# Kernel tuning notes

Hardware: AMD Instinct MI355X
Metric: run time of the kernel (lower is better)

The kernel has to match this reference:

```python
import jax, jax.numpy as jnp
import numpy as np

N_NODES = 10000
N_EDGES = 640000
D_FEAT = 128


def setup_inputs() -> dict:
    key = jax.random.key(0)
    k1, k2, k3, k4 = jax.random.split(key, 4)
    feat = jax.random.normal(k1, (N_NODES, D_FEAT), dtype=jnp.float32)
    src = jax.random.randint(k2, (N_EDGES,), 0, N_NODES, dtype=jnp.int32)
    dst = jax.random.randint(k3, (N_EDGES,), 0, N_NODES, dtype=jnp.int32)
    W = jax.random.normal(k4, (D_FEAT, D_FEAT), dtype=jnp.float32) / np.sqrt(D_FEAT).astype(np.float32)
    b = jnp.zeros((D_FEAT,), dtype=jnp.float32)
    return {"feat": feat, "W": W, "b": b, "src": src, "dst": dst}


def reference(feat, W, b, src, dst):
    eps = jnp.float32(0.0)  # init_eps=0, learn_eps=False (buffer)
    n = feat.shape[0]
    # message passing: copy_u('h','m') + sum reducer -> neigh[i] = sum_{j->i} h_j
    h_src = feat[src]                                   # [E, D] gather
    neigh = jax.ops.segment_sum(h_src, dst, num_segments=n)  # [N, D] scatter-add
    rst = (1.0 + eps) * feat + neigh
    # apply_func: Linear(D, D)
    rst = rst @ W + b
    # per-edge score: e = sum(h_src * tanh(h_dst), axis=1)
    e = jnp.sum(h_src * jnp.tanh(feat[dst]), axis=1)    # [E]
    # edge_softmax: softmax over edges grouped by destination node
    m = jax.ops.segment_max(e, dst, num_segments=n)     # [N]
    e_exp = jnp.exp(e - m[dst])
    denom = jax.ops.segment_sum(e_exp, dst, num_segments=n)  # [N]
    e_soft = e_exp / denom[dst]
    return rst, e_soft
```

## Files before the change

kernel.cpp:

```cpp
#include <hip/hip_runtime.h>
#include <hip/hip_bf16.h>
#include <math.h>

#define N_NODES 10000
#define N_EDGES 640000
#define D_FEAT  128
#define SLOT    128
#define MAXDEG  128


__device__ __forceinline__ unsigned bf16rne2(float a, float b) {
    unsigned ua = __float_as_uint(a);
    unsigned ub = __float_as_uint(b);
    unsigned ra = (ua + 0x7fffu + ((ua >> 16) & 1u)) >> 16;
    unsigned rb = (ub + 0x7fffu + ((ub >> 16) & 1u)) >> 16;
    return ra | (rb << 16);
}

__global__ void scatter_build(const int* __restrict__ src,
                              const int* __restrict__ dst,
                              const float* __restrict__ feat,
                              int* __restrict__ cnt,
                              unsigned short* __restrict__ slot_us,
                              int* __restrict__ pos_by_edge,
                              unsigned short* __restrict__ feat_bf) {
    int tid = blockIdx.x * 256 + threadIdx.x;

    if (tid < (N_NODES * D_FEAT) / 8) {
        int t8 = tid * 8;
        float4 f0 = *(const float4*)&feat[t8];
        float4 f1 = *(const float4*)&feat[t8 + 4];
        uint4 p;
        p.x = bf16rne2(f0.x, f0.y);
        p.y = bf16rne2(f0.z, f0.w);
        p.z = bf16rne2(f1.x, f1.y);
        p.w = bf16rne2(f1.z, f1.w);
        *(uint4*)&feat_bf[t8] = p;
    }

    int d = dst[tid];
    int s = src[tid];
    int pos = atomicAdd(&cnt[d << 4], 1);
    int idx = d * SLOT + pos;
    slot_us[idx] = (unsigned short)s;
    pos_by_edge[tid] = idx;
}

__device__ __forceinline__ float cvt_acc_dot(uint4 U, float4 t0, float4 t1,
                                             float4& a0, float4& a1) {
    float v0 = __uint_as_float(U.x << 16);
    float v1 = __uint_as_float(U.x & 0xffff0000u);
    float v2 = __uint_as_float(U.y << 16);
    float v3 = __uint_as_float(U.y & 0xffff0000u);
    float v4 = __uint_as_float(U.z << 16);
    float v5 = __uint_as_float(U.z & 0xffff0000u);
    float v6 = __uint_as_float(U.w << 16);
    float v7 = __uint_as_float(U.w & 0xffff0000u);
    a0.x += v0; a0.y += v1; a0.z += v2; a0.w += v3;
    a1.x += v4; a1.y += v5; a1.z += v6; a1.w += v7;
    return v0 * t0.x + v1 * t0.y + v2 * t0.z + v3 * t0.w
         + v4 * t1.x + v5 * t1.y + v6 * t1.z + v7 * t1.w;
}

__global__ void fused_node(const float* __restrict__ feat,
                           const unsigned short* __restrict__ feat_bf,
                           const int* __restrict__ cnt,
                           const unsigned short* __restrict__ slot_us,
                           float* __restrict__ e_slot,
                           float* __restrict__ x_out) {
    __shared__ float t_sh[4][D_FEAT];
    __shared__ float e_sh[4][MAXDEG];
    int wv = threadIdx.x >> 6;
    int lane = threadIdx.x & 63;
    int node = blockIdx.x * 4 + wv;
    if (node >= N_NODES) return;

    int g = lane >> 4;
    int l = lane & 15;

    int deg = cnt[node << 4];
    int dm = (deg > 0) ? deg - 1 : 0;
    unsigned base = (unsigned)node * SLOT;

    float2 fd2 = ((const float2*)(feat + (size_t)node * D_FEAT))[lane];
    ((float2*)&t_sh[wv][0])[lane] = make_float2(tanhf(fd2.x), tanhf(fd2.y));
    float4 t0 = ((const float4*)&t_sh[wv][0])[l * 2];
    float4 t1 = ((const float4*)&t_sh[wv][0])[l * 2 + 1];

    int m0 = (int)slot_us[base + min(lane, dm)];
    int m1 = (int)slot_us[base + min(64 + lane, dm)];

    float4 acc0 = make_float4(0.f, 0.f, 0.f, 0.f);
    float4 acc1 = make_float4(0.f, 0.f, 0.f, 0.f);

    int nsteps = (deg + 7) >> 3;

    uint4 Ua0, Ua1;
    #define LOAD_STEP(T, U0, U1)                                              \
        {                                                                     \
            int m_ = ((T) < 8) ? m0 : m1;                                     \
            int s0_ = __shfl(m_, ((T) * 8 + g) & 63, 64);                     \
            int s1_ = __shfl(m_, ((T) * 8 + 4 + g) & 63, 64);                 \
            U0 = *((const uint4*)(feat_bf + (size_t)s0_ * D_FEAT) + l);       \
            U1 = *((const uint4*)(feat_bf + (size_t)s1_ * D_FEAT) + l);       \
        }

    if (nsteps > 0) LOAD_STEP(0, Ua0, Ua1);

    for (int t = 0; t < nsteps; ++t) {
        uint4 Ub0 = Ua0, Ub1 = Ua1;
        if (t + 1 < nsteps) LOAD_STEP(t + 1, Ub0, Ub1);

        int i0 = t * 8 + g;
        int i1 = i0 + 4;
        if (((t + 1) << 3) <= deg) {
            float d0 = cvt_acc_dot(Ua0, t0, t1, acc0, acc1);
            float d1 = cvt_acc_dot(Ua1, t0, t1, acc0, acc1);
            #pragma unroll
            for (int off = 1; off <= 8; off <<= 1) {
                d0 += __shfl_xor(d0, off, 64);
                d1 += __shfl_xor(d1, off, 64);
            }
            if (l == 0) {
                e_sh[wv][i0] = d0;
                e_sh[wv][i1] = d1;
            }
        } else {
            bool a0 = i0 < deg, a1 = i1 < deg;
            if (!a0) Ua0 = make_uint4(0u, 0u, 0u, 0u);
            if (!a1) Ua1 = make_uint4(0u, 0u, 0u, 0u);
            float d0 = cvt_acc_dot(Ua0, t0, t1, acc0, acc1);
            float d1 = cvt_acc_dot(Ua1, t0, t1, acc0, acc1);
            #pragma unroll
            for (int off = 1; off <= 8; off <<= 1) {
                d0 += __shfl_xor(d0, off, 64);
                d1 += __shfl_xor(d1, off, 64);
            }
            if (a0 && l == 0) e_sh[wv][i0] = d0;
            if (a1 && l == 0) e_sh[wv][i1] = d1;
        }
        Ua0 = Ub0; Ua1 = Ub1;
    }
    #undef LOAD_STEP

    #pragma unroll
    for (int off = 16; off <= 32; off <<= 1) {
        acc0.x += __shfl_xor(acc0.x, off, 64);
        acc0.y += __shfl_xor(acc0.y, off, 64);
        acc0.z += __shfl_xor(acc0.z, off, 64);
        acc0.w += __shfl_xor(acc0.w, off, 64);
        acc1.x += __shfl_xor(acc1.x, off, 64);
        acc1.y += __shfl_xor(acc1.y, off, 64);
        acc1.z += __shfl_xor(acc1.z, off, 64);
        acc1.w += __shfl_xor(acc1.w, off, 64);
    }

    float2 mp = (g == 0) ? make_float2(acc0.x, acc0.y)
              : (g == 1) ? make_float2(acc0.z, acc0.w)
              : (g == 2) ? make_float2(acc1.x, acc1.y)
              :            make_float2(acc1.z, acc1.w);
    int p2 = l * 4 + g;
    float2 fn = ((const float2*)(feat + (size_t)node * D_FEAT))[p2];
    ((float2*)(x_out + (size_t)node * D_FEAT))[p2] =
        make_float2(mp.x + fn.x, mp.y + fn.y);

    float mx = -INFINITY;
    for (int i = lane; i < deg; i += 64) mx = fmaxf(mx, e_sh[wv][i]);
    #pragma unroll
    for (int off = 32; off; off >>= 1)
        mx = fmaxf(mx, __shfl_xor(mx, off, 64));

    float sum = 0.f;
    for (int i = lane; i < deg; i += 64) {
        float ex = expf(e_sh[wv][i] - mx);
        e_sh[wv][i] = ex;
        sum += ex;
    }
    #pragma unroll
    for (int off = 32; off; off >>= 1)
        sum += __shfl_xor(sum, off, 64);

    float inv = 1.0f / sum;
    for (int i = lane; i < deg; i += 64)
        e_slot[base + i] = e_sh[wv][i] * inv;
}

__global__ void gemm_and_edge(float* __restrict__ io,
                              const float* __restrict__ W,
                              const float* __restrict__ b,
                              const int* __restrict__ pos_by_edge,
                              const float* __restrict__ e_slot,
                              float* __restrict__ out_e) {
    if (blockIdx.x >= 625) {
        int i4 = ((blockIdx.x - 625) * 256 + threadIdx.x) * 4;
        int4 p = *(const int4*)&pos_by_edge[i4];
        float4 r;
        r.x = e_slot[p.x];
        r.y = e_slot[p.y];
        r.z = e_slot[p.z];
        r.w = e_slot[p.w];
        *(float4*)&out_e[i4] = r;
        return;
    }

    __shared__ float xst[D_FEAT][20];
    int rbase = blockIdx.x * 16;

    for (int i = threadIdx.x; i < 16 * D_FEAT; i += 256) {
        int r = i >> 7, c = i & 127;
        xst[c][r] = io[(size_t)(rbase + r) * D_FEAT + c];
    }
    __syncthreads();

    int tc = threadIdx.x & 63;
    int rh = threadIdx.x >> 6;
    float a00 = 0.f, a01 = 0.f, a10 = 0.f, a11 = 0.f;
    float a20 = 0.f, a21 = 0.f, a30 = 0.f, a31 = 0.f;

    for (int k = 0; k < D_FEAT; ++k) {
        float2 xa = *(const float2*)&xst[k][rh * 4];
        float2 xb = *(const float2*)&xst[k][rh * 4 + 2];
        float2 w  = *(const float2*)&W[(size_t)k * D_FEAT + tc * 2];
        a00 += xa.x * w.x; a01 += xa.x * w.y;
        a10 += xa.y * w.x; a11 += xa.y * w.y;
        a20 += xb.x * w.x; a21 += xb.x * w.y;
        a30 += xb.y * w.x; a31 += xb.y * w.y;
    }
    __syncthreads();

    float2 bias = *(const float2*)&b[tc * 2];
    int rw = rbase + rh * 4;
    ((float2*)&io[(size_t)(rw + 0) * D_FEAT])[tc] = make_float2(a00 + bias.x, a01 + bias.y);
    ((float2*)&io[(size_t)(rw + 1) * D_FEAT])[tc] = make_float2(a10 + bias.x, a11 + bias.y);
    ((float2*)&io[(size_t)(rw + 2) * D_FEAT])[tc] = make_float2(a20 + bias.x, a21 + bias.y);
    ((float2*)&io[(size_t)(rw + 3) * D_FEAT])[tc] = make_float2(a30 + bias.x, a31 + bias.y);
}

extern "C" void kernel_launch(void* const* d_in, const int* in_sizes, int n_in,
                              void* d_out, int out_size, void* d_ws, size_t ws_size,
                              hipStream_t stream) {
    const float* feat = (const float*)d_in[0];
    const float* W    = (const float*)d_in[1];
    const float* b    = (const float*)d_in[2];
    const int*   src  = (const int*)d_in[3];
    const int*   dst  = (const int*)d_in[4];

    float* out_rst = (float*)d_out;
    float* out_e   = (float*)d_out + (size_t)N_NODES * D_FEAT;

    char* ws = (char*)d_ws;
    int*            cnt         = (int*)(ws + 0);
    unsigned short* slot_us     = (unsigned short*)(ws + 640000);
    float*          e_slot      = (float*)(ws + 3200000);
    int*            pos_by_edge = (int*)(ws + 8320000);
    unsigned short* feat_bf     = (unsigned short*)(ws + 10880000);

    hipMemsetAsync(cnt, 0, 640000, stream);

    scatter_build<<<N_EDGES / 256, 256, 0, stream>>>(src, dst, feat, cnt,
                                                     slot_us, pos_by_edge, feat_bf);

    fused_node<<<(N_NODES + 3) / 4, 256, 0, stream>>>(feat, feat_bf, cnt,
                                                      slot_us, e_slot, out_rst);

    gemm_and_edge<<<1250, 256, 0, stream>>>(out_rst, W, b, pos_by_edge, e_slot, out_e);
}
```

Baseline: 136.7 us.

## Partition per-node edge counters and slots by XCD to localize atomics

```diff
diff --git a/kernel.cpp b/kernel.cpp
--- a/kernel.cpp
+++ b/kernel.cpp
@@ -5,7 +5,8 @@
 #define N_NODES 10000
 #define N_EDGES 640000
 #define D_FEAT  128
-#define SLOT    128
+#define NXCD    8
+#define SEG     64
 #define MAXDEG  128
 
 
@@ -38,10 +39,14 @@
         *(uint4*)&feat_bf[t8] = p;
     }
 
+    unsigned xcd;
+    asm volatile("s_getreg_b32 %0, hwreg(HW_REG_XCC_ID)" : "=s"(xcd));
+    xcd &= 7;
+
     int d = dst[tid];
     int s = src[tid];
-    int pos = atomicAdd(&cnt[d << 4], 1);
-    int idx = d * SLOT + pos;
+    int pos = atomicAdd(&cnt[xcd * 16384 + d], 1);
+    int idx = d * (NXCD * SEG) + xcd * SEG + pos;
     slot_us[idx] = (unsigned short)s;
     pos_by_edge[tid] = idx;
 }
@@ -70,6 +75,7 @@
                            float* __restrict__ x_out) {
     __shared__ float t_sh[4][D_FEAT];
     __shared__ float e_sh[4][MAXDEG];
+    __shared__ unsigned short src_sh[4][MAXDEG];
     int wv = threadIdx.x >> 6;
     int lane = threadIdx.x & 63;
     int node = blockIdx.x * 4 + wv;
@@ -78,17 +84,32 @@
     int g = lane >> 4;
     int l = lane & 15;
 
-    int deg = cnt[node << 4];
+    unsigned sbase = (unsigned)node * (NXCD * SEG);
+
+    int cme = (lane < NXCD) ? cnt[lane * 16384 + node] : 0;
+    int cg[NXCD], psum[NXCD + 1];
+    psum[0] = 0;
+    #pragma unroll
+    for (int k = 0; k < NXCD; ++k) {
+        cg[k] = __shfl(cme, k, 64);
+        psum[k + 1] = psum[k] + cg[k];
+    }
+    int deg = psum[NXCD];
+    #pragma unroll
+    for (int k = 0; k < NXCD; ++k) {
+        if (lane < cg[k])
+            src_sh[wv][psum[k] + lane] = slot_us[sbase + k * SEG + lane];
+    }
+
     int dm = (deg > 0) ? deg - 1 : 0;
-    unsigned base = (unsigned)node * SLOT;
 
     float2 fd2 = ((const float2*)(feat + (size_t)node * D_FEAT))[lane];
     ((float2*)&t_sh[wv][0])[lane] = make_float2(tanhf(fd2.x), tanhf(fd2.y));
     float4 t0 = ((const float4*)&t_sh[wv][0])[l * 2];
     float4 t1 = ((const float4*)&t_sh[wv][0])[l * 2 + 1];
 
-    int m0 = (int)slot_us[base + min(lane, dm)];
-    int m1 = (int)slot_us[base + min(64 + lane, dm)];
+    int m0 = (int)src_sh[wv][min(lane, dm)];
+    int m1 = (int)src_sh[wv][min(64 + lane, dm)];
 
     float4 acc0 = make_float4(0.f, 0.f, 0.f, 0.f);
     float4 acc1 = make_float4(0.f, 0.f, 0.f, 0.f);
@@ -181,8 +202,11 @@
         sum += __shfl_xor(sum, off, 64);
 
     float inv = 1.0f / sum;
-    for (int i = lane; i < deg; i += 64)
-        e_slot[base + i] = e_sh[wv][i] * inv;
+    #pragma unroll
+    for (int k = 0; k < NXCD; ++k) {
+        if (lane < cg[k])
+            e_slot[sbase + k * SEG + lane] = e_sh[wv][psum[k] + lane] * inv;
+    }
 }
 
 __global__ void gemm_and_edge(float* __restrict__ io,
@@ -250,12 +274,12 @@
 
     char* ws = (char*)d_ws;
     int*            cnt         = (int*)(ws + 0);
-    unsigned short* slot_us     = (unsigned short*)(ws + 640000);
-    float*          e_slot      = (float*)(ws + 3200000);
-    int*            pos_by_edge = (int*)(ws + 8320000);
-    unsigned short* feat_bf     = (unsigned short*)(ws + 10880000);
-
-    hipMemsetAsync(cnt, 0, 640000, stream);
+    unsigned short* slot_us     = (unsigned short*)(ws + 524288);
+    float*          e_slot      = (float*)(ws + 10764288);
+    int*            pos_by_edge = (int*)(ws + 31244288);
+    unsigned short* feat_bf     = (unsigned short*)(ws + 33804288);
+
+    hipMemsetAsync(cnt, 0, NXCD * 16384 * sizeof(int), stream);
 
     scatter_build<<<N_EDGES / 256, 256, 0, stream>>>(src, dst, feat, cnt,
                                                      slot_us, pos_by_edge, feat_bf);
```

Result: slower. 156.5 us (+14.5%).
